# Kernel tuning notes

Hardware: AMD Instinct MI355X
Metric: run time of the kernel (lower is better)

Reference implementation:

```python
import jax, jax.numpy as jnp
import numpy as np

NUM_LAYER = 5
HIDDEN = 128
PROJ = 256
ATOM_VOCAB = 128
BOND_VOCAB = 16
N_ATOM_FEATS = 9
N_BOND_FEATS = 3
BN_EPS = 1e-5


def _batchnorm(x, gamma, beta):
    # training-mode BatchNorm1d over the node axis
    mu = x.mean(axis=0)
    var = x.var(axis=0)
    return (x - mu) * jax.lax.rsqrt(var + BN_EPS) * gamma + beta


def setup_inputs() -> dict:
    key = jax.random.key(0)
    ks = jax.random.split(key, 16)
    N, E = 40000, 640000
    s = 0.05
    inp = {
        "x": jax.random.randint(ks[0], (N, N_ATOM_FEATS), 0, ATOM_VOCAB, dtype=jnp.int32),
        "edge_index": jax.random.randint(ks[1], (2, E), 0, N, dtype=jnp.int32),
        "edge_attr": jax.random.randint(ks[2], (E, N_BOND_FEATS), 0, BOND_VOCAB, dtype=jnp.int32),
        "atom_emb": jax.random.normal(ks[3], (N_ATOM_FEATS, ATOM_VOCAB, HIDDEN), jnp.float32) * s,
        "bond_emb": jax.random.normal(ks[4], (NUM_LAYER, N_BOND_FEATS, BOND_VOCAB, HIDDEN), jnp.float32) * s,
        "eps": jnp.zeros((NUM_LAYER,), jnp.float32),
        "w1": jax.random.normal(ks[5], (NUM_LAYER, HIDDEN, 2 * HIDDEN), jnp.float32) * s,
        "b1": jnp.zeros((NUM_LAYER, 2 * HIDDEN), jnp.float32),
        "bn1_g": jnp.ones((NUM_LAYER, 2 * HIDDEN), jnp.float32),
        "bn1_b": jnp.zeros((NUM_LAYER, 2 * HIDDEN), jnp.float32),
        "w2": jax.random.normal(ks[6], (NUM_LAYER, 2 * HIDDEN, HIDDEN), jnp.float32) * s,
        "b2": jnp.zeros((NUM_LAYER, HIDDEN), jnp.float32),
        "bn_g": jnp.ones((NUM_LAYER, HIDDEN), jnp.float32),
        "bn_b": jnp.zeros((NUM_LAYER, HIDDEN), jnp.float32),
        "lin_w": jax.random.normal(ks[7], (HIDDEN, PROJ), jnp.float32) * s,
        "lin_b": jnp.zeros((PROJ,), jnp.float32),
    }
    return inp


def reference(x, edge_index, edge_attr, atom_emb, bond_emb, eps, w1, b1, bn1_g, bn1_b, w2, b2, bn_g, bn_b, lin_w, lin_b):
    N = x.shape[0]
    src, dst = edge_index[0], edge_index[1]
    # AtomEncoder: sum of per-column embeddings -> [N, H]
    h = atom_emb[jnp.arange(N_ATOM_FEATS), x].sum(axis=1)
    for l in range(NUM_LAYER):
        # BondEncoder for this layer -> [E, H]
        e = bond_emb[l][jnp.arange(N_BOND_FEATS), edge_attr].sum(axis=1)
        # message: relu(x_j + edge_emb); aggregate: scatter-add to dst
        msg = jax.nn.relu(h[src] + e)
        agg = jax.ops.segment_sum(msg, dst, num_segments=N)
        z = (1.0 + eps[l]) * h + agg
        # GIN MLP: Linear -> BN -> ReLU -> Linear
        z = z @ w1[l] + b1[l]
        z = jax.nn.relu(_batchnorm(z, bn1_g[l], bn1_b[l]))
        z = z @ w2[l] + b2[l]
        # outer BatchNorm, relu except last layer
        h = _batchnorm(z, bn_g[l], bn_b[l])
        if l < NUM_LAYER - 1:
            h = jax.nn.relu(h)
    return h @ lin_w + lin_b
```

## Files before the change

kernel.cpp:

```cpp
#include <hip/hip_runtime.h>
#include <stdint.h>


typedef unsigned short ushort_t;
typedef unsigned int uint_t;
typedef __attribute__((ext_vector_type(8))) short bf16x8;
typedef __attribute__((ext_vector_type(16))) float f32x16;

#define MFMA32(a, b, c) __builtin_amdgcn_mfma_f32_32x32x16_bf16(a, b, c, 0, 0, 0)

__device__ inline ushort_t f2bf(float f) {
  uint_t u = __builtin_bit_cast(uint_t, f);
  u += 0x7FFFu + ((u >> 16) & 1u);
  return (ushort_t)(u >> 16);
}
__device__ inline float bf2f(uint_t h) {
  uint_t u = (h & 0xFFFFu) << 16;
  return __builtin_bit_cast(float, u);
}
__device__ inline uint_t pack2(float a, float b) {
  return (uint_t)f2bf(a) | ((uint_t)f2bf(b) << 16);
}
__device__ inline f32x16 zero16() {
  f32x16 z;
#pragma unroll
  for (int i = 0; i < 16; ++i) z[i] = 0.f;
  return z;
}


__global__ __launch_bounds__(256) void bond_comb_k(
    const float* __restrict__ bemb, ushort_t* __restrict__ comb)
{
  int idx = blockIdx.x * 256 + threadIdx.x;
  if (idx >= 5 * 4096 * 64) return;
  int lane = idx & 63, c = (idx >> 6) & 4095, l = idx >> 18;
  const float2* b2 = (const float2*)(bemb + (size_t)l * 3 * 16 * 128);
  float2 e0 = b2[(c & 15) * 64 + lane];
  float2 e1 = b2[(16 + ((c >> 4) & 15)) * 64 + lane];
  float2 e2 = b2[(32 + (c >> 8)) * 64 + lane];
  ((uint_t*)comb)[idx] = pack2(e0.x + e1.x + e2.x, e0.y + e1.y + e2.y);
}

__global__ __launch_bounds__(256) void swz_all_k(
    const float* __restrict__ w1, const float* __restrict__ linw,
    const float* __restrict__ w2, ushort_t* __restrict__ bswz1,
    ushort_t* __restrict__ bswz2)
{
  int t = blockIdx.x * 256 + threadIdx.x;
  if (t >= 11 * 4096) return;
  int m = t >> 12, tt = t & 4095, lane = tt & 63;
  if (m < 6) {
    const float* w = (m < 5) ? (w1 + (size_t)m * 32768) : linw;
    ushort_t* o = bswz1 + (size_t)m * 32768;
    int nt = (tt >> 6) & 7, s = tt >> 9;
    int kb = s * 16 + (lane >> 5) * 8, n = nt * 32 + (lane & 31);
    ushort_t tmp[8];
#pragma unroll
    for (int j = 0; j < 8; ++j) tmp[j] = f2bf(w[(size_t)(kb + j) * 256 + n]);
    ((uint4*)o)[tt] = *(uint4*)tmp;
  } else {
    int mm = m - 6;
    const float* w = w2 + (size_t)mm * 32768;
    ushort_t* o = bswz2 + (size_t)mm * 32768;
    int nt = (tt >> 6) & 3, s = tt >> 8;
    int kb = s * 16 + (lane >> 5) * 8, n = nt * 32 + (lane & 31);
    ushort_t tmp[8];
#pragma unroll
    for (int j = 0; j < 8; ++j) tmp[j] = f2bf(w[(size_t)(kb + j) * 128 + n]);
    ((uint4*)o)[tt] = *(uint4*)tmp;
  }
}


__global__ void zero_int_k(int* p, int n) {
  int i = blockIdx.x * 256 + threadIdx.x;
  if (i < n) p[i] = 0;
}

__global__ void hist_k(const int* __restrict__ ei, int* __restrict__ cnt, int E) {
  int e = blockIdx.x * 256 + threadIdx.x;
  if (e >= E) return;
  atomicAdd(&cnt[ei[E + e]], 1);
}

__global__ __launch_bounds__(256) void block_sum_k(
    const int* __restrict__ cnt, int* __restrict__ bsum, int N)
{
  __shared__ int red[256];
  int t = threadIdx.x, idx = blockIdx.x * 256 + t;
  red[t] = (idx < N) ? cnt[idx] : 0;
  __syncthreads();
  for (int o = 128; o > 0; o >>= 1) {
    if (t < o) red[t] += red[t + o];
    __syncthreads();
  }
  if (t == 0) bsum[blockIdx.x] = red[0];
}

__global__ __launch_bounds__(256) void scan_bsum_k(
    int* __restrict__ bsum, int* __restrict__ rsN, int nb)
{
  __shared__ int s[256];
  int t = threadIdx.x;
  s[t] = (t < nb) ? bsum[t] : 0;
  __syncthreads();
  for (int o = 1; o < 256; o <<= 1) {
    int v = (t >= o) ? s[t - o] : 0;
    __syncthreads();
    s[t] += v;
    __syncthreads();
  }
  if (t < nb) bsum[t] = (t == 0) ? 0 : s[t - 1];
  if (t == nb - 1) *rsN = s[t];
}

__global__ __launch_bounds__(256) void scan_write_k(
    const int* __restrict__ cnt, const int* __restrict__ bsum,
    int* __restrict__ rs, int* __restrict__ cursor, int N)
{
  __shared__ int s[256];
  int t = threadIdx.x, idx = blockIdx.x * 256 + t;
  int v = (idx < N) ? cnt[idx] : 0;
  s[t] = v;
  __syncthreads();
  for (int o = 1; o < 256; o <<= 1) {
    int u = (t >= o) ? s[t - o] : 0;
    __syncthreads();
    s[t] += u;
    __syncthreads();
  }
  int excl = s[t] - v + bsum[blockIdx.x];
  if (idx < N) { rs[idx] = excl; cursor[idx] = excl; }
}

__global__ void scatter_k(const int* __restrict__ ei, const int* __restrict__ ea,
                          int* __restrict__ cursor, uint32_t* __restrict__ sorted, int E)
{
  int e = blockIdx.x * 256 + threadIdx.x;
  if (e >= E) return;
  int src = ei[e], dst = ei[E + e];
  int a0 = ea[e * 3], a1 = ea[e * 3 + 1], a2 = ea[e * 3 + 2];
  int pos = atomicAdd(&cursor[dst], 1);
  sorted[pos] = (uint32_t)src | ((uint32_t)a0 << 16) | ((uint32_t)a1 << 20) | ((uint32_t)a2 << 24);
}


__global__ __launch_bounds__(256) void atom_encode_k(
    const int* __restrict__ x, const float* __restrict__ aemb,
    ushort_t* __restrict__ hbn, int N)
{
  int idx = blockIdx.x * 256 + threadIdx.x;
  if (idx >= N * 64) return;
  int n = idx >> 6, lane = idx & 63;
  const int* xr = x + n * 9;
  float sx = 0.f, sy = 0.f;
#pragma unroll
  for (int f = 0; f < 9; ++f) {
    float2 e = ((const float2*)(aemb + (size_t)(f * 128 + xr[f]) * 128))[lane];
    sx += e.x; sy += e.y;
  }
  ((uint_t*)hbn)[idx] = pack2(sx, sy);
}

__global__ __launch_bounds__(256) void bnrelu_k(
    const float* __restrict__ raw, const float* __restrict__ stats2,
    const float* __restrict__ g, const float* __restrict__ bb,
    ushort_t* __restrict__ hbn, float invN, int total)
{
  int t = blockIdx.x * 256 + threadIdx.x;
  int lane = t & 63;
  int c0 = 2 * lane, c1 = c0 + 1;
  float mu0 = stats2[c0] * invN, mu1 = stats2[c1] * invN;
  float v0 = stats2[128 + c0] * invN - mu0 * mu0;
  float v1 = stats2[128 + c1] * invN - mu1 * mu1;
  float scx = rsqrtf(v0 + 1e-5f) * g[c0];
  float scy = rsqrtf(v1 + 1e-5f) * g[c1];
  float shx = bb[c0] - mu0 * scx;
  float shy = bb[c1] - mu1 * scy;
  int stride = gridDim.x * 256;
  for (int idx = t; idx < total; idx += stride) {
    float2 h = ((const float2*)raw)[idx];
    float hx = fmaxf(fmaf(h.x, scx, shx), 0.f);
    float hy = fmaxf(fmaf(h.y, scy, shy), 0.f);
    ((uint_t*)hbn)[idx] = pack2(hx, hy);
  }
}

__global__ __launch_bounds__(256) void aggregate_k(
    const ushort_t* __restrict__ hbn, const ushort_t* __restrict__ comb,
    const uint32_t* __restrict__ sorted, const int* __restrict__ rs,
    const float* __restrict__ eps, int layer, ushort_t* __restrict__ zin,
    float* __restrict__ stats, int N)
{
  if (blockIdx.x == 0) {
    stats[threadIdx.x] = 0.f;
    stats[threadIdx.x + 256] = 0.f;
  }
  int wave = threadIdx.x >> 6, lane = threadIdx.x & 63;
  int n = blockIdx.x * 4 + wave;
  if (n >= N) return;
  int beg = rs[n], end = rs[n + 1];
  const uint_t* hb = (const uint_t*)hbn;
  const uint_t* cb = ((const uint_t*)comb) + (size_t)layer * 4096 * 64;
  float ax = 0.f, ay = 0.f;
  int i = beg;
  for (; i + 16 <= end; i += 16) {
    uint32_t p[16];
#pragma unroll
    for (int j = 0; j < 16; ++j) p[j] = sorted[i + j];
    uint_t hv[16], ee[16];
#pragma unroll
    for (int j = 0; j < 16; ++j) {
      hv[j] = hb[(size_t)(p[j] & 0xFFFFu) * 64 + lane];
      ee[j] = cb[(p[j] >> 16) * 64 + lane];
    }
#pragma unroll
    for (int j = 0; j < 16; ++j) {
      ax += fmaxf(bf2f(hv[j]) + bf2f(ee[j]), 0.f);
      ay += fmaxf(bf2f(hv[j] >> 16) + bf2f(ee[j] >> 16), 0.f);
    }
  }
  for (; i + 4 <= end; i += 4) {
    uint32_t p[4];
#pragma unroll
    for (int j = 0; j < 4; ++j) p[j] = sorted[i + j];
    uint_t hv[4], ee[4];
#pragma unroll
    for (int j = 0; j < 4; ++j) {
      hv[j] = hb[(size_t)(p[j] & 0xFFFFu) * 64 + lane];
      ee[j] = cb[(p[j] >> 16) * 64 + lane];
    }
#pragma unroll
    for (int j = 0; j < 4; ++j) {
      ax += fmaxf(bf2f(hv[j]) + bf2f(ee[j]), 0.f);
      ay += fmaxf(bf2f(hv[j] >> 16) + bf2f(ee[j] >> 16), 0.f);
    }
  }
  for (; i < end; ++i) {
    uint32_t p = sorted[i];
    uint_t ee = cb[(p >> 16) * 64 + lane];
    uint_t hv = hb[(size_t)(p & 0xFFFFu) * 64 + lane];
    ax += fmaxf(bf2f(hv) + bf2f(ee), 0.f);
    ay += fmaxf(bf2f(hv >> 16) + bf2f(ee >> 16), 0.f);
  }
  float s = 1.f + eps[layer];
  uint_t hn = hb[(size_t)n * 64 + lane];
  ((uint_t*)zin)[(size_t)n * 64 + lane] =
      pack2(fmaf(s, bf2f(hn), ax), fmaf(s, bf2f(hn >> 16), ay));
}


__global__ __launch_bounds__(256) void gemm1_stats_k(
    const ushort_t* __restrict__ in, const ushort_t* __restrict__ bswz,
    const float* __restrict__ bias, float* __restrict__ statsOut,
    float* __restrict__ zeroPtr)
{
  __shared__ ushort_t As[64 * 128];
  int tid = threadIdx.x;
  int wave = tid >> 6, lane = tid & 63;
  int lr = lane & 31, half = lane >> 5;
  int row0 = blockIdx.x * 64;
  if (blockIdx.x == 0) zeroPtr[tid] = 0.f;
  {
    const uint2* src = (const uint2*)(in + (size_t)row0 * 128);
#pragma unroll
    for (int i = 0; i < 8; ++i) {
      int idx = tid + 256 * i;
      int r = idx >> 5, c = (idx & 31) * 4;
      uint2 v = src[idx];
      int scol = (((c >> 3) ^ (r & 15)) << 3) | (c & 7);
      *(uint2*)&As[r * 128 + scol] = v;
    }
  }
  __syncthreads();
  int nt0 = wave * 2, nt1 = nt0 + 1;
  f32x16 acc00 = zero16(), acc01 = zero16(), acc10 = zero16(), acc11 = zero16();
  const bf16x8* Bp = (const bf16x8*)bswz;
#pragma unroll
  for (int s = 0; s < 8; ++s) {
    int k = s * 16 + half * 8;
    int scol = ((k >> 3) ^ (lr & 15)) << 3;
    bf16x8 a0 = *(const bf16x8*)&As[lr * 128 + scol];
    bf16x8 a1 = *(const bf16x8*)&As[(32 + lr) * 128 + scol];
    bf16x8 b0 = Bp[(s * 8 + nt0) * 64 + lane];
    bf16x8 b1 = Bp[(s * 8 + nt1) * 64 + lane];
    acc00 = MFMA32(a0, b0, acc00);
    acc10 = MFMA32(a1, b0, acc10);
    acc01 = MFMA32(a0, b1, acc01);
    acc11 = MFMA32(a1, b1, acc11);
  }
  int col0 = nt0 * 32 + lr, col1 = nt1 * 32 + lr;
  float bv0 = bias[col0], bv1 = bias[col1];
  float s0 = 0, q0 = 0, s1 = 0, q1 = 0;
#pragma unroll
  for (int r2 = 0; r2 < 16; ++r2) {
    float v00 = acc00[r2] + bv0, v10 = acc10[r2] + bv0;
    float v01 = acc01[r2] + bv1, v11 = acc11[r2] + bv1;
    s0 += v00 + v10; q0 += v00 * v00 + v10 * v10;
    s1 += v01 + v11; q1 += v01 * v01 + v11 * v11;
  }
  s0 += __shfl_xor(s0, 32); q0 += __shfl_xor(q0, 32);
  s1 += __shfl_xor(s1, 32); q1 += __shfl_xor(q1, 32);
  if (lane < 32) {
    atomicAdd(&statsOut[col0], s0);
    atomicAdd(&statsOut[256 + col0], q0);
    atomicAdd(&statsOut[col1], s1);
    atomicAdd(&statsOut[256 + col1], q1);
  }
}

__global__ __launch_bounds__(256) void fused_mlp_k(
    const ushort_t* __restrict__ in, const ushort_t* __restrict__ bswz1,
    const float* __restrict__ b1, const float* __restrict__ stats1,
    const float* __restrict__ g1, const float* __restrict__ bb1,
    const ushort_t* __restrict__ bswz2, const float* __restrict__ b2,
    float* __restrict__ outf, float* __restrict__ stats2, float invN)
{
  __shared__ ushort_t As[64 * 128];
  __shared__ ushort_t Bs[64 * 256];
  __shared__ float sc1[256], sh1[256];
  int tid = threadIdx.x;
  int wave = tid >> 6, lane = tid & 63;
  int lr = lane & 31, half = lane >> 5;
  int row0 = blockIdx.x * 64;
  {
    int c = tid;
    float mu = stats1[c] * invN;
    float var = stats1[256 + c] * invN - mu * mu;
    float r = rsqrtf(var + 1e-5f) * g1[c];
    sc1[c] = r;
    sh1[c] = bb1[c] - mu * r + b1[c] * r;
  }
  {
    const uint2* src = (const uint2*)(in + (size_t)row0 * 128);
#pragma unroll
    for (int i = 0; i < 8; ++i) {
      int idx = tid + 256 * i;
      int r = idx >> 5, c = (idx & 31) * 4;
      uint2 v = src[idx];
      int scol = (((c >> 3) ^ (r & 15)) << 3) | (c & 7);
      *(uint2*)&As[r * 128 + scol] = v;
    }
  }
  __syncthreads();
  int nt0 = wave * 2, nt1 = nt0 + 1;
  f32x16 acc00 = zero16(), acc01 = zero16(), acc10 = zero16(), acc11 = zero16();
  {
    const bf16x8* Bp = (const bf16x8*)bswz1;
#pragma unroll
    for (int s = 0; s < 8; ++s) {
      int k = s * 16 + half * 8;
      int scol = ((k >> 3) ^ (lr & 15)) << 3;
      bf16x8 a0 = *(const bf16x8*)&As[lr * 128 + scol];
      bf16x8 a1 = *(const bf16x8*)&As[(32 + lr) * 128 + scol];
      bf16x8 b0v = Bp[(s * 8 + nt0) * 64 + lane];
      bf16x8 b1v = Bp[(s * 8 + nt1) * 64 + lane];
      acc00 = MFMA32(a0, b0v, acc00);
      acc10 = MFMA32(a1, b0v, acc10);
      acc01 = MFMA32(a0, b1v, acc01);
      acc11 = MFMA32(a1, b1v, acc11);
    }
  }
  {
    int col0 = nt0 * 32 + lr, col1 = nt1 * 32 + lr;
    float sc0v = sc1[col0], sh0v = sh1[col0];
    float sc1v = sc1[col1], sh1v = sh1[col1];
    auto wr = [&](const f32x16& a, int mtb, int col, float scv, float shv) {
#pragma unroll
      for (int r2 = 0; r2 < 16; ++r2) {
        int row = mtb + (r2 & 3) + 8 * (r2 >> 2) + 4 * half;
        float v = fmaxf(fmaf(a[r2], scv, shv), 0.f);
        int scol = (((col >> 3) ^ (row & 15)) << 3) | (col & 7);
        Bs[row * 256 + scol] = f2bf(v);
      }
    };
    wr(acc00, 0, col0, sc0v, sh0v);
    wr(acc10, 32, col0, sc0v, sh0v);
    wr(acc01, 0, col1, sc1v, sh1v);
    wr(acc11, 32, col1, sc1v, sh1v);
  }
  __syncthreads();
  f32x16 acc0 = zero16(), acc1 = zero16();
  {
    const bf16x8* Bp2 = (const bf16x8*)bswz2;
#pragma unroll
    for (int s = 0; s < 16; ++s) {
      int k = s * 16 + half * 8;
      int scol = ((k >> 3) ^ (lr & 15)) << 3;
      bf16x8 a0 = *(const bf16x8*)&Bs[lr * 256 + scol];
      bf16x8 a1 = *(const bf16x8*)&Bs[(32 + lr) * 256 + scol];
      bf16x8 b = Bp2[(s * 4 + wave) * 64 + lane];
      acc0 = MFMA32(a0, b, acc0);
      acc1 = MFMA32(a1, b, acc1);
    }
  }
  int col = wave * 32 + lr;
  float bv = b2[col];
  float s0 = 0, q0 = 0;
  auto emit = [&](const f32x16& a, int mtb) {
#pragma unroll
    for (int r2 = 0; r2 < 16; ++r2) {
      int row = row0 + mtb + (r2 & 3) + 8 * (r2 >> 2) + 4 * half;
      float v = a[r2] + bv;
      outf[(size_t)row * 128 + col] = v;
      s0 += v;
      q0 += v * v;
    }
  };
  emit(acc0, 0);
  emit(acc1, 32);
  s0 += __shfl_xor(s0, 32);
  q0 += __shfl_xor(q0, 32);
  if (lane < 32) {
    atomicAdd(&stats2[col], s0);
    atomicAdd(&stats2[128 + col], q0);
  }
}

__global__ __launch_bounds__(256) void final_proj_k(
    const float* __restrict__ inf, const ushort_t* __restrict__ bswz,
    const float* __restrict__ bias, const float* __restrict__ stats2,
    const float* __restrict__ g, const float* __restrict__ bb,
    float* __restrict__ outf, float invN)
{
  __shared__ ushort_t As[64 * 128];
  __shared__ float sc[128], sh[128];
  int tid = threadIdx.x;
  int wave = tid >> 6, lane = tid & 63;
  int lr = lane & 31, half = lane >> 5;
  int row0 = blockIdx.x * 64;
  if (tid < 128) {
    int c = tid;
    float mu = stats2[c] * invN;
    float var = stats2[128 + c] * invN - mu * mu;
    float r = rsqrtf(var + 1e-5f) * g[c];
    sc[c] = r;
    sh[c] = bb[c] - mu * r;
  }
  __syncthreads();
  {
    const float4* src = (const float4*)(inf + (size_t)row0 * 128);
#pragma unroll
    for (int i = 0; i < 8; ++i) {
      int idx = tid + 256 * i;
      int r = idx >> 5, c = (idx & 31) * 4;
      float4 v = src[idx];
      v.x = fmaf(v.x, sc[c], sh[c]);
      v.y = fmaf(v.y, sc[c + 1], sh[c + 1]);
      v.z = fmaf(v.z, sc[c + 2], sh[c + 2]);
      v.w = fmaf(v.w, sc[c + 3], sh[c + 3]);
      uint2 o;
      o.x = pack2(v.x, v.y);
      o.y = pack2(v.z, v.w);
      int scol = (((c >> 3) ^ (r & 15)) << 3) | (c & 7);
      *(uint2*)&As[r * 128 + scol] = o;
    }
  }
  __syncthreads();
  int nt0 = wave * 2, nt1 = nt0 + 1;
  f32x16 acc00 = zero16(), acc01 = zero16(), acc10 = zero16(), acc11 = zero16();
  const bf16x8* Bp = (const bf16x8*)bswz;
#pragma unroll
  for (int s = 0; s < 8; ++s) {
    int k = s * 16 + half * 8;
    int scol = ((k >> 3) ^ (lr & 15)) << 3;
    bf16x8 a0 = *(const bf16x8*)&As[lr * 128 + scol];
    bf16x8 a1 = *(const bf16x8*)&As[(32 + lr) * 128 + scol];
    bf16x8 b0 = Bp[(s * 8 + nt0) * 64 + lane];
    bf16x8 b1 = Bp[(s * 8 + nt1) * 64 + lane];
    acc00 = MFMA32(a0, b0, acc00);
    acc10 = MFMA32(a1, b0, acc10);
    acc01 = MFMA32(a0, b1, acc01);
    acc11 = MFMA32(a1, b1, acc11);
  }
  int col0 = nt0 * 32 + lr, col1 = nt1 * 32 + lr;
  float bv0 = bias[col0], bv1 = bias[col1];
  auto emit = [&](const f32x16& a, int mtb, int col, float bv) {
#pragma unroll
    for (int r2 = 0; r2 < 16; ++r2) {
      int row = row0 + mtb + (r2 & 3) + 8 * (r2 >> 2) + 4 * half;
      outf[(size_t)row * 256 + col] = a[r2] + bv;
    }
  };
  emit(acc00, 0, col0, bv0);
  emit(acc10, 32, col0, bv0);
  emit(acc01, 0, col1, bv1);
  emit(acc11, 32, col1, bv1);
}

extern "C" void kernel_launch(void* const* d_in, const int* in_sizes, int n_in,
                              void* d_out, int out_size, void* d_ws, size_t ws_size,
                              hipStream_t stream)
{
  const int* x = (const int*)d_in[0];
  const int* ei = (const int*)d_in[1];
  const int* ea = (const int*)d_in[2];
  const float* aemb = (const float*)d_in[3];
  const float* bemb = (const float*)d_in[4];
  const float* eps = (const float*)d_in[5];
  const float* w1 = (const float*)d_in[6];
  const float* b1 = (const float*)d_in[7];
  const float* bn1g = (const float*)d_in[8];
  const float* bn1b = (const float*)d_in[9];
  const float* w2 = (const float*)d_in[10];
  const float* b2 = (const float*)d_in[11];
  const float* bng = (const float*)d_in[12];
  const float* bnb = (const float*)d_in[13];
  const float* linw = (const float*)d_in[14];
  const float* linb = (const float*)d_in[15];
  int N = in_sizes[0] / 9;
  int E = in_sizes[1] / 2;
  int nb = (N + 255) / 256;

  char* ws = (char*)d_ws;
  size_t off = 0;
  auto alloc = [&](size_t bytes) {
    void* p = ws + off;
    off += (bytes + 255) & ~(size_t)255;
    return p;
  };
  float* raw = (float*)alloc((size_t)N * 128 * 4);
  ushort_t* hbn = (ushort_t*)alloc((size_t)N * 128 * 2);
  ushort_t* zin = (ushort_t*)alloc((size_t)N * 128 * 2);
  ushort_t* comb = (ushort_t*)alloc((size_t)5 * 4096 * 128 * 2);
  ushort_t* bswz1 = (ushort_t*)alloc((size_t)6 * 32768 * 2);
  ushort_t* bswz2 = (ushort_t*)alloc((size_t)5 * 32768 * 2);
  uint32_t* sorted = (uint32_t*)alloc((size_t)E * 4);
  int* rs = (int*)alloc((size_t)(N + 1) * 4);
  int* cursor = (int*)alloc((size_t)N * 4);
  int* cnt = (int*)alloc((size_t)N * 4);
  int* bsum = (int*)alloc((size_t)nb * 4);
  float* stats = (float*)alloc(768 * 4);
  float invN = 1.f / (float)N;

  bond_comb_k<<<(5 * 4096 * 64 + 255) / 256, 256, 0, stream>>>(bemb, comb);
  swz_all_k<<<(11 * 4096 + 255) / 256, 256, 0, stream>>>(w1, linw, w2, bswz1, bswz2);

  atom_encode_k<<<(N * 64 + 255) / 256, 256, 0, stream>>>(x, aemb, hbn, N);
  zero_int_k<<<(N + 255) / 256, 256, 0, stream>>>(cnt, N);
  hist_k<<<(E + 255) / 256, 256, 0, stream>>>(ei, cnt, E);
  block_sum_k<<<nb, 256, 0, stream>>>(cnt, bsum, N);
  scan_bsum_k<<<1, 256, 0, stream>>>(bsum, rs + N, nb);
  scan_write_k<<<nb, 256, 0, stream>>>(cnt, bsum, rs, cursor, N);
  scatter_k<<<(E + 255) / 256, 256, 0, stream>>>(ei, ea, cursor, sorted, E);

  for (int l = 0; l < 5; ++l) {
    if (l > 0) {
      bnrelu_k<<<2048, 256, 0, stream>>>(
          raw, stats + 512, bng + (size_t)(l - 1) * 128,
          bnb + (size_t)(l - 1) * 128, hbn, invN, N * 64);
    }
    aggregate_k<<<(N + 3) / 4, 256, 0, stream>>>(
        hbn, comb, sorted, rs, eps, l, zin, stats, N);
    gemm1_stats_k<<<N / 64, 256, 0, stream>>>(
        zin, bswz1 + (size_t)l * 32768, b1 + (size_t)l * 256,
        stats, stats + 512);
    fused_mlp_k<<<N / 64, 256, 0, stream>>>(
        zin, bswz1 + (size_t)l * 32768, b1 + (size_t)l * 256,
        stats, bn1g + (size_t)l * 256, bn1b + (size_t)l * 256,
        bswz2 + (size_t)l * 32768, b2 + (size_t)l * 128,
        raw, stats + 512, invN);
  }
  final_proj_k<<<N / 64, 256, 0, stream>>>(
      raw, bswz1 + (size_t)5 * 32768, linb, stats + 512,
      bng + (size_t)4 * 128, bnb + (size_t)4 * 128, (float*)d_out, invN);
}
```

Baseline: 626.1 us.

## Fuse neighbor aggregation with first GEMM and store bf16 intermediate instead of recomputing

Merges the aggregation kernel with the first MLP GEMM: each 512-thread block aggregates 64 nodes straight into shared memory and runs the GEMM there, so the zin round trip through global memory goes away. The aggregate is kept as a hi/lo bf16 split, which doubles the MFMA count to preserve precision. The first GEMM output is written as bf16 into the raw buffer, so the second kernel no longer recomputes GEMM1 and only applies BN+ReLU before GEMM2. Stats zeroing moves to the atom encode and bnrelu kernels. The costs are an extra bf16 rounding of the pre-BN activations and an in-place aliasing of the raw buffer between the two kernels.

Result: no change. 622.7 us (-0.5%).

```diff
diff --git a/kernel.cpp b/kernel.cpp
--- a/kernel.cpp
+++ b/kernel.cpp
@@ -148,8 +148,12 @@
 
 __global__ __launch_bounds__(256) void atom_encode_k(
     const int* __restrict__ x, const float* __restrict__ aemb,
-    ushort_t* __restrict__ hbn, int N)
-{
+    ushort_t* __restrict__ hbn, float* __restrict__ stats, int N)
+{
+  if (blockIdx.x == 0) {
+    stats[threadIdx.x] = 0.f;
+    stats[threadIdx.x + 256] = 0.f;
+  }
   int idx = blockIdx.x * 256 + threadIdx.x;
   if (idx >= N * 64) return;
   int n = idx >> 6, lane = idx & 63;
@@ -166,8 +170,13 @@
 __global__ __launch_bounds__(256) void bnrelu_k(
     const float* __restrict__ raw, const float* __restrict__ stats2,
     const float* __restrict__ g, const float* __restrict__ bb,
-    ushort_t* __restrict__ hbn, float invN, int total)
-{
+    ushort_t* __restrict__ hbn, float* __restrict__ statsZero,
+    float invN, int total)
+{
+  if (blockIdx.x == 0) {
+    statsZero[threadIdx.x] = 0.f;
+    statsZero[threadIdx.x + 256] = 0.f;
+  }
   int t = blockIdx.x * 256 + threadIdx.x;
   int lane = t & 63;
   int c0 = 2 * lane, c1 = c0 + 1;
@@ -187,137 +196,124 @@
   }
 }
 
-__global__ __launch_bounds__(256) void aggregate_k(
+__global__ __launch_bounds__(512, 4) void agg_gemm1_k(
     const ushort_t* __restrict__ hbn, const ushort_t* __restrict__ comb,
     const uint32_t* __restrict__ sorted, const int* __restrict__ rs,
-    const float* __restrict__ eps, int layer, ushort_t* __restrict__ zin,
-    float* __restrict__ stats, int N)
-{
-  if (blockIdx.x == 0) {
-    stats[threadIdx.x] = 0.f;
-    stats[threadIdx.x + 256] = 0.f;
-  }
-  int wave = threadIdx.x >> 6, lane = threadIdx.x & 63;
-  int n = blockIdx.x * 4 + wave;
-  if (n >= N) return;
-  int beg = rs[n], end = rs[n + 1];
+    const float* __restrict__ eps, int layer,
+    const ushort_t* __restrict__ bswz, const float* __restrict__ bias,
+    ushort_t* __restrict__ z1bf, float* __restrict__ stats, int N)
+{
+  __shared__ ushort_t As[64 * 128];
+  __shared__ ushort_t Al[64 * 128];
+  int tid = threadIdx.x;
+  int wave = tid >> 6, lane = tid & 63;
+  int row0 = blockIdx.x * 64;
+  if (blockIdx.x == 0 && tid < 256) stats[512 + tid] = 0.f;
   const uint_t* hb = (const uint_t*)hbn;
   const uint_t* cb = ((const uint_t*)comb) + (size_t)layer * 4096 * 64;
-  float ax = 0.f, ay = 0.f;
-  int i = beg;
-  for (; i + 16 <= end; i += 16) {
-    uint32_t p[16];
-#pragma unroll
-    for (int j = 0; j < 16; ++j) p[j] = sorted[i + j];
-    uint_t hv[16], ee[16];
-#pragma unroll
-    for (int j = 0; j < 16; ++j) {
-      hv[j] = hb[(size_t)(p[j] & 0xFFFFu) * 64 + lane];
-      ee[j] = cb[(p[j] >> 16) * 64 + lane];
-    }
-#pragma unroll
-    for (int j = 0; j < 16; ++j) {
-      ax += fmaxf(bf2f(hv[j]) + bf2f(ee[j]), 0.f);
-      ay += fmaxf(bf2f(hv[j] >> 16) + bf2f(ee[j] >> 16), 0.f);
-    }
-  }
-  for (; i + 4 <= end; i += 4) {
-    uint32_t p[4];
-#pragma unroll
-    for (int j = 0; j < 4; ++j) p[j] = sorted[i + j];
-    uint_t hv[4], ee[4];
-#pragma unroll
-    for (int j = 0; j < 4; ++j) {
-      hv[j] = hb[(size_t)(p[j] & 0xFFFFu) * 64 + lane];
-      ee[j] = cb[(p[j] >> 16) * 64 + lane];
-    }
-#pragma unroll
-    for (int j = 0; j < 4; ++j) {
-      ax += fmaxf(bf2f(hv[j]) + bf2f(ee[j]), 0.f);
-      ay += fmaxf(bf2f(hv[j] >> 16) + bf2f(ee[j] >> 16), 0.f);
-    }
-  }
-  for (; i < end; ++i) {
-    uint32_t p = sorted[i];
-    uint_t ee = cb[(p >> 16) * 64 + lane];
-    uint_t hv = hb[(size_t)(p & 0xFFFFu) * 64 + lane];
-    ax += fmaxf(bf2f(hv) + bf2f(ee), 0.f);
-    ay += fmaxf(bf2f(hv >> 16) + bf2f(ee >> 16), 0.f);
-  }
-  float s = 1.f + eps[layer];
-  uint_t hn = hb[(size_t)n * 64 + lane];
-  ((uint_t*)zin)[(size_t)n * 64 + lane] =
-      pack2(fmaf(s, bf2f(hn), ax), fmaf(s, bf2f(hn >> 16), ay));
-}
-
-
-__global__ __launch_bounds__(256) void gemm1_stats_k(
-    const ushort_t* __restrict__ in, const ushort_t* __restrict__ bswz,
-    const float* __restrict__ bias, float* __restrict__ statsOut,
-    float* __restrict__ zeroPtr)
-{
-  __shared__ ushort_t As[64 * 128];
-  int tid = threadIdx.x;
-  int wave = tid >> 6, lane = tid & 63;
+  float s_eps = 1.f + eps[layer];
+#pragma unroll 1
+  for (int j = 0; j < 8; ++j) {
+    int r = wave + 8 * j;
+    int n = row0 + r;
+    int beg = rs[n], end = rs[n + 1];
+    float ax = 0.f, ay = 0.f;
+    int i = beg;
+    for (; i + 16 <= end; i += 16) {
+      uint32_t p[16];
+#pragma unroll
+      for (int jj = 0; jj < 16; ++jj) p[jj] = sorted[i + jj];
+      uint_t hv[16], ee[16];
+#pragma unroll
+      for (int jj = 0; jj < 16; ++jj) {
+        hv[jj] = hb[(size_t)(p[jj] & 0xFFFFu) * 64 + lane];
+        ee[jj] = cb[(p[jj] >> 16) * 64 + lane];
+      }
+#pragma unroll
+      for (int jj = 0; jj < 16; ++jj) {
+        ax += fmaxf(bf2f(hv[jj]) + bf2f(ee[jj]), 0.f);
+        ay += fmaxf(bf2f(hv[jj] >> 16) + bf2f(ee[jj] >> 16), 0.f);
+      }
+    }
+    for (; i + 4 <= end; i += 4) {
+      uint32_t p[4];
+#pragma unroll
+      for (int jj = 0; jj < 4; ++jj) p[jj] = sorted[i + jj];
+      uint_t hv[4], ee[4];
+#pragma unroll
+      for (int jj = 0; jj < 4; ++jj) {
+        hv[jj] = hb[(size_t)(p[jj] & 0xFFFFu) * 64 + lane];
+        ee[jj] = cb[(p[jj] >> 16) * 64 + lane];
+      }
+#pragma unroll
+      for (int jj = 0; jj < 4; ++jj) {
+        ax += fmaxf(bf2f(hv[jj]) + bf2f(ee[jj]), 0.f);
+        ay += fmaxf(bf2f(hv[jj] >> 16) + bf2f(ee[jj] >> 16), 0.f);
+      }
+    }
+    for (; i < end; ++i) {
+      uint32_t p = sorted[i];
+      uint_t ee = cb[(p >> 16) * 64 + lane];
+      uint_t hv = hb[(size_t)(p & 0xFFFFu) * 64 + lane];
+      ax += fmaxf(bf2f(hv) + bf2f(ee), 0.f);
+      ay += fmaxf(bf2f(hv >> 16) + bf2f(ee >> 16), 0.f);
+    }
+    uint_t hn = hb[(size_t)n * 64 + lane];
+    float zx = fmaf(s_eps, bf2f(hn), ax);
+    float zy = fmaf(s_eps, bf2f(hn >> 16), ay);
+    ushort_t hxz = f2bf(zx), hyz = f2bf(zy);
+    float lox = zx - bf2f(hxz), loy = zy - bf2f(hyz);
+    int c = 2 * lane;
+    int scol = (((c >> 3) ^ (r & 15)) << 3) | (c & 7);
+    *(uint_t*)&As[r * 128 + scol] = (uint_t)hxz | ((uint_t)hyz << 16);
+    *(uint_t*)&Al[r * 128 + scol] = pack2(lox, loy);
+  }
+  __syncthreads();
   int lr = lane & 31, half = lane >> 5;
-  int row0 = blockIdx.x * 64;
-  if (blockIdx.x == 0) zeroPtr[tid] = 0.f;
-  {
-    const uint2* src = (const uint2*)(in + (size_t)row0 * 128);
-#pragma unroll
-    for (int i = 0; i < 8; ++i) {
-      int idx = tid + 256 * i;
-      int r = idx >> 5, c = (idx & 31) * 4;
-      uint2 v = src[idx];
-      int scol = (((c >> 3) ^ (r & 15)) << 3) | (c & 7);
-      *(uint2*)&As[r * 128 + scol] = v;
-    }
-  }
-  __syncthreads();
-  int nt0 = wave * 2, nt1 = nt0 + 1;
-  f32x16 acc00 = zero16(), acc01 = zero16(), acc10 = zero16(), acc11 = zero16();
+  int nt = wave;
+  f32x16 acc0 = zero16(), acc1 = zero16();
   const bf16x8* Bp = (const bf16x8*)bswz;
 #pragma unroll
   for (int s = 0; s < 8; ++s) {
     int k = s * 16 + half * 8;
     int scol = ((k >> 3) ^ (lr & 15)) << 3;
-    bf16x8 a0 = *(const bf16x8*)&As[lr * 128 + scol];
-    bf16x8 a1 = *(const bf16x8*)&As[(32 + lr) * 128 + scol];
-    bf16x8 b0 = Bp[(s * 8 + nt0) * 64 + lane];
-    bf16x8 b1 = Bp[(s * 8 + nt1) * 64 + lane];
-    acc00 = MFMA32(a0, b0, acc00);
-    acc10 = MFMA32(a1, b0, acc10);
-    acc01 = MFMA32(a0, b1, acc01);
-    acc11 = MFMA32(a1, b1, acc11);
-  }
-  int col0 = nt0 * 32 + lr, col1 = nt1 * 32 + lr;
-  float bv0 = bias[col0], bv1 = bias[col1];
-  float s0 = 0, q0 = 0, s1 = 0, q1 = 0;
+    bf16x8 b = Bp[(s * 8 + nt) * 64 + lane];
+    bf16x8 ah0 = *(const bf16x8*)&As[lr * 128 + scol];
+    bf16x8 al0 = *(const bf16x8*)&Al[lr * 128 + scol];
+    bf16x8 ah1 = *(const bf16x8*)&As[(32 + lr) * 128 + scol];
+    bf16x8 al1 = *(const bf16x8*)&Al[(32 + lr) * 128 + scol];
+    acc0 = MFMA32(ah0, b, acc0);
+    acc0 = MFMA32(al0, b, acc0);
+    acc1 = MFMA32(ah1, b, acc1);
+    acc1 = MFMA32(al1, b, acc1);
+  }
+  int col = nt * 32 + lr;
+  float bv = bias[col];
+  float s0 = 0.f, q0 = 0.f;
 #pragma unroll
   for (int r2 = 0; r2 < 16; ++r2) {
-    float v00 = acc00[r2] + bv0, v10 = acc10[r2] + bv0;
-    float v01 = acc01[r2] + bv1, v11 = acc11[r2] + bv1;
-    s0 += v00 + v10; q0 += v00 * v00 + v10 * v10;
-    s1 += v01 + v11; q1 += v01 * v01 + v11 * v11;
-  }
-  s0 += __shfl_xor(s0, 32); q0 += __shfl_xor(q0, 32);
-  s1 += __shfl_xor(s1, 32); q1 += __shfl_xor(q1, 32);
+    int rrow = (r2 & 3) + 8 * (r2 >> 2) + 4 * half;
+    float v0 = acc0[r2] + bv;
+    float v1 = acc1[r2] + bv;
+    z1bf[(size_t)(row0 + rrow) * 256 + col] = f2bf(v0);
+    z1bf[(size_t)(row0 + 32 + rrow) * 256 + col] = f2bf(v1);
+    s0 += v0 + v1;
+    q0 += v0 * v0 + v1 * v1;
+  }
+  s0 += __shfl_xor(s0, 32);
+  q0 += __shfl_xor(q0, 32);
   if (lane < 32) {
-    atomicAdd(&statsOut[col0], s0);
-    atomicAdd(&statsOut[256 + col0], q0);
-    atomicAdd(&statsOut[col1], s1);
-    atomicAdd(&statsOut[256 + col1], q1);
-  }
-}
-
-__global__ __launch_bounds__(256) void fused_mlp_k(
-    const ushort_t* __restrict__ in, const ushort_t* __restrict__ bswz1,
-    const float* __restrict__ b1, const float* __restrict__ stats1,
+    atomicAdd(&stats[col], s0);
+    atomicAdd(&stats[256 + col], q0);
+  }
+}
+
+__global__ __launch_bounds__(256) void mlp2_k(
+    float* rawz, const float* __restrict__ stats1,
     const float* __restrict__ g1, const float* __restrict__ bb1,
     const ushort_t* __restrict__ bswz2, const float* __restrict__ b2,
-    float* __restrict__ outf, float* __restrict__ stats2, float invN)
-{
-  __shared__ ushort_t As[64 * 128];
+    float* __restrict__ stats2, float invN)
+{
   __shared__ ushort_t Bs[64 * 256];
   __shared__ float sc1[256], sh1[256];
   int tid = threadIdx.x;
@@ -325,60 +321,36 @@
   int lr = lane & 31, half = lane >> 5;
   int row0 = blockIdx.x * 64;
   {
-    int c = tid;
-    float mu = stats1[c] * invN;
-    float var = stats1[256 + c] * invN - mu * mu;
-    float r = rsqrtf(var + 1e-5f) * g1[c];
-    sc1[c] = r;
-    sh1[c] = bb1[c] - mu * r + b1[c] * r;
-  }
+    float mu = stats1[tid] * invN;
+    float var = stats1[256 + tid] * invN - mu * mu;
+    float r = rsqrtf(var + 1e-5f) * g1[tid];
+    sc1[tid] = r;
+    sh1[tid] = bb1[tid] - mu * r;
+  }
+  __syncthreads();
   {
-    const uint2* src = (const uint2*)(in + (size_t)row0 * 128);
+    const uint4* src = (const uint4*)((const ushort_t*)rawz + (size_t)row0 * 256);
 #pragma unroll
     for (int i = 0; i < 8; ++i) {
       int idx = tid + 256 * i;
-      int r = idx >> 5, c = (idx & 31) * 4;
-      uint2 v = src[idx];
-      int scol = (((c >> 3) ^ (r & 15)) << 3) | (c & 7);
-      *(uint2*)&As[r * 128 + scol] = v;
-    }
-  }
-  __syncthreads();
-  int nt0 = wave * 2, nt1 = nt0 + 1;
-  f32x16 acc00 = zero16(), acc01 = zero16(), acc10 = zero16(), acc11 = zero16();
-  {
-    const bf16x8* Bp = (const bf16x8*)bswz1;
-#pragma unroll
-    for (int s = 0; s < 8; ++s) {
-      int k = s * 16 + half * 8;
-      int scol = ((k >> 3) ^ (lr & 15)) << 3;
-      bf16x8 a0 = *(const bf16x8*)&As[lr * 128 + scol];
-      bf16x8 a1 = *(const bf16x8*)&As[(32 + lr) * 128 + scol];
-      bf16x8 b0v = Bp[(s * 8 + nt0) * 64 + lane];
-      bf16x8 b1v = Bp[(s * 8 + nt1) * 64 + lane];
-      acc00 = MFMA32(a0, b0v, acc00);
-      acc10 = MFMA32(a1, b0v, acc10);
-      acc01 = MFMA32(a0, b1v, acc01);
-      acc11 = MFMA32(a1, b1v, acc11);
-    }
-  }
-  {
-    int col0 = nt0 * 32 + lr, col1 = nt1 * 32 + lr;
-    float sc0v = sc1[col0], sh0v = sh1[col0];
-    float sc1v = sc1[col1], sh1v = sh1[col1];
-    auto wr = [&](const f32x16& a, int mtb, int col, float scv, float shv) {
-#pragma unroll
-      for (int r2 = 0; r2 < 16; ++r2) {
-        int row = mtb + (r2 & 3) + 8 * (r2 >> 2) + 4 * half;
-        float v = fmaxf(fmaf(a[r2], scv, shv), 0.f);
-        int scol = (((col >> 3) ^ (row & 15)) << 3) | (col & 7);
-        Bs[row * 256 + scol] = f2bf(v);
-      }
-    };
-    wr(acc00, 0, col0, sc0v, sh0v);
-    wr(acc10, 32, col0, sc0v, sh0v);
-    wr(acc01, 0, col1, sc1v, sh1v);
-    wr(acc11, 32, col1, sc1v, sh1v);
+      int r = idx >> 5, c = (idx & 31) * 8;
+      uint4 v = src[idx];
+      float f0 = fmaxf(fmaf(bf2f(v.x), sc1[c], sh1[c]), 0.f);
+      float f1 = fmaxf(fmaf(bf2f(v.x >> 16), sc1[c + 1], sh1[c + 1]), 0.f);
+      float f2 = fmaxf(fmaf(bf2f(v.y), sc1[c + 2], sh1[c + 2]), 0.f);
+      float f3 = fmaxf(fmaf(bf2f(v.y >> 16), sc1[c + 3], sh1[c + 3]), 0.f);
+      float f4 = fmaxf(fmaf(bf2f(v.z), sc1[c + 4], sh1[c + 4]), 0.f);
+      float f5 = fmaxf(fmaf(bf2f(v.z >> 16), sc1[c + 5], sh1[c + 5]), 0.f);
+      float f6 = fmaxf(fmaf(bf2f(v.w), sc1[c + 6], sh1[c + 6]), 0.f);
+      float f7 = fmaxf(fmaf(bf2f(v.w >> 16), sc1[c + 7], sh1[c + 7]), 0.f);
+      uint4 o;
+      o.x = pack2(f0, f1);
+      o.y = pack2(f2, f3);
+      o.z = pack2(f4, f5);
+      o.w = pack2(f6, f7);
+      int scol = ((c >> 3) ^ (r & 15)) << 3;
+      *(uint4*)&Bs[r * 256 + scol] = o;
+    }
   }
   __syncthreads();
   f32x16 acc0 = zero16(), acc1 = zero16();
@@ -397,13 +369,13 @@
   }
   int col = wave * 32 + lr;
   float bv = b2[col];
-  float s0 = 0, q0 = 0;
+  float s0 = 0.f, q0 = 0.f;
   auto emit = [&](const f32x16& a, int mtb) {
 #pragma unroll
     for (int r2 = 0; r2 < 16; ++r2) {
       int row = row0 + mtb + (r2 & 3) + 8 * (r2 >> 2) + 4 * half;
       float v = a[r2] + bv;
-      outf[(size_t)row * 128 + col] = v;
+      rawz[(size_t)row * 128 + col] = v;
       s0 += v;
       q0 += v * v;
     }
@@ -522,7 +494,6 @@
   };
   float* raw = (float*)alloc((size_t)N * 128 * 4);
   ushort_t* hbn = (ushort_t*)alloc((size_t)N * 128 * 2);
-  ushort_t* zin = (ushort_t*)alloc((size_t)N * 128 * 2);
   ushort_t* comb = (ushort_t*)alloc((size_t)5 * 4096 * 128 * 2);
   ushort_t* bswz1 = (ushort_t*)alloc((size_t)6 * 32768 * 2);
   ushort_t* bswz2 = (ushort_t*)alloc((size_t)5 * 32768 * 2);
@@ -537,7 +508,7 @@
   bond_comb_k<<<(5 * 4096 * 64 + 255) / 256, 256, 0, stream>>>(bemb, comb);
   swz_all_k<<<(11 * 4096 + 255) / 256, 256, 0, stream>>>(w1, linw, w2, bswz1, bswz2);
 
-  atom_encode_k<<<(N * 64 + 255) / 256, 256, 0, stream>>>(x, aemb, hbn, N);
+  atom_encode_k<<<(N * 64 + 255) / 256, 256, 0, stream>>>(x, aemb, hbn, stats, N);
   zero_int_k<<<(N + 255) / 256, 256, 0, stream>>>(cnt, N);
   hist_k<<<(E + 255) / 256, 256, 0, stream>>>(ei, cnt, E);
   block_sum_k<<<nb, 256, 0, stream>>>(cnt, bsum, N);
@@ -549,18 +520,16 @@
     if (l > 0) {
       bnrelu_k<<<2048, 256, 0, stream>>>(
           raw, stats + 512, bng + (size_t)(l - 1) * 128,
-          bnb + (size_t)(l - 1) * 128, hbn, invN, N * 64);
-    }
-    aggregate_k<<<(N + 3) / 4, 256, 0, stream>>>(
-        hbn, comb, sorted, rs, eps, l, zin, stats, N);
-    gemm1_stats_k<<<N / 64, 256, 0, stream>>>(
-        zin, bswz1 + (size_t)l * 32768, b1 + (size_t)l * 256,
-        stats, stats + 512);
-    fused_mlp_k<<<N / 64, 256, 0, stream>>>(
-        zin, bswz1 + (size_t)l * 32768, b1 + (size_t)l * 256,
-        stats, bn1g + (size_t)l * 256, bn1b + (size_t)l * 256,
+          bnb + (size_t)(l - 1) * 128, hbn, stats, invN, N * 64);
+    }
+    agg_gemm1_k<<<N / 64, 512, 0, stream>>>(
+        hbn, comb, sorted, rs, eps, l,
+        bswz1 + (size_t)l * 32768, b1 + (size_t)l * 256,
+        (ushort_t*)raw, stats, N);
+    mlp2_k<<<N / 64, 256, 0, stream>>>(
+        raw, stats, bn1g + (size_t)l * 256, bn1b + (size_t)l * 256,
         bswz2 + (size_t)l * 32768, b2 + (size_t)l * 128,
-        raw, stats + 512, invN);
+        stats + 512, invN);
   }
   final_proj_k<<<N / 64, 256, 0, stream>>>(
       raw, bswz1 + (size_t)5 * 32768, linb, stats + 512,
```
